# Optimization experiments

Hardware: AMD Instinct MI355X
Metric: run time of the kernel (lower is better)

## Reference

```python
import jax, jax.numpy as jnp
import numpy as np

D_MODEL = 1024
N_HEADS = 16
D_HEAD = D_MODEL // N_HEADS
B, T = 4, 2048


def setup_inputs() -> dict:
    key = jax.random.key(0)
    k1, k2, k3 = jax.random.split(key, 3)
    x = jax.random.normal(k1, (B, T, D_MODEL), dtype=jnp.float32)
    # match nn.Linear init scale roughly (uniform ~ 1/sqrt(fan_in)); scale normal for stability
    w_qkv = jax.random.normal(k2, (D_MODEL, 3 * D_MODEL), dtype=jnp.float32) / np.sqrt(D_MODEL)
    w_out = jax.random.normal(k3, (D_MODEL, D_MODEL), dtype=jnp.float32) / np.sqrt(D_MODEL)
    return {"x": x, "w_qkv": w_qkv, "w_out": w_out}


def reference(x, w_qkv, w_out):
    Bx, Tx, D = x.shape
    H, Dh = N_HEADS, D_HEAD
    qkv = x @ w_qkv                                  # [B,T,3D]
    qkv = qkv.reshape(Bx, Tx, 3, H, Dh)
    q, k, v = qkv[:, :, 0], qkv[:, :, 1], qkv[:, :, 2]  # [B,T,H,Dh]
    scores = jnp.einsum('bqhd,bkhd->bhqk', q, k) / np.sqrt(Dh).astype(np.float32)
    mask = jnp.triu(jnp.ones((Tx, Tx), dtype=bool), k=1)  # causal: mask future
    scores = jnp.where(mask, -jnp.inf, scores)
    attn = jax.nn.softmax(scores, axis=-1)
    out = jnp.einsum('bhqk,bkhd->bqhd', attn, v).reshape(Bx, Tx, D)
    return out @ w_out
```

## Files before the change

### kernel.cpp

```cpp
#include <hip/hip_runtime.h>
#include <math.h>

#define T_SEQ 2048
#define NB 4
#define NH 16
#define DH 64
#define DM 1024

typedef __attribute__((ext_vector_type(8))) __bf16 bf16x8;
typedef __attribute__((ext_vector_type(4))) float f32x4;

typedef const __attribute__((address_space(1))) void* gas_t;
typedef __attribute__((address_space(3))) void* las_t;

#if __has_builtin(__builtin_amdgcn_exp2f)
#define EXP2(x) __builtin_amdgcn_exp2f(x)
#else
#define EXP2(x) __expf((x) * 0.69314718056f)
#endif

#define SCHED0 __builtin_amdgcn_sched_barrier(0)
#define GLD(src, dst) __builtin_amdgcn_global_load_lds((gas_t)(src), (las_t)(dst), 16, 0, 0)
#define WAIT_VM(N) asm volatile("s_waitcnt vmcnt(" #N ")" ::: "memory")
#define WAIT_LGKM0 asm volatile("s_waitcnt lgkmcnt(0)" ::: "memory")
#define MEMFENCE   asm volatile("" ::: "memory")

__device__ inline bool detect_f32(const unsigned short* probe, int lane) {
    unsigned short u = probe[lane];
    int e = (u >> 7) & 0xFF;
    bool outlier = (e >= 140) || (e <= 90 && (u & 0x7fff) != 0);
    unsigned long long m = __ballot(outlier);
    return __popcll(m) >= 4;
}

__device__ inline bf16x8 load8_flex(const void* base, long elem, bool f32) {
    if (!f32) {
        return *(const bf16x8*)((const __bf16*)base + elem);
    } else {
        const float* f = (const float*)base + elem;
        float4 a = *(const float4*)f;
        float4 b = *(const float4*)(f + 4);
        bf16x8 r;
        r[0] = (__bf16)a.x; r[1] = (__bf16)a.y; r[2] = (__bf16)a.z; r[3] = (__bf16)a.w;
        r[4] = (__bf16)b.x; r[5] = (__bf16)b.y; r[6] = (__bf16)b.z; r[7] = (__bf16)b.w;
        return r;
    }
}

__global__ __launch_bounds__(256)
void cvt_x(const float* __restrict__ in, __bf16* __restrict__ out, long n8) {
    long i = (long)blockIdx.x * blockDim.x + threadIdx.x;
    if (i >= n8) return;
    const float* f = in + i * 8;
    float4 a = *(const float4*)f;
    float4 b = *(const float4*)(f + 4);
    bf16x8 r;
    r[0] = (__bf16)a.x; r[1] = (__bf16)a.y; r[2] = (__bf16)a.z; r[3] = (__bf16)a.w;
    r[4] = (__bf16)b.x; r[5] = (__bf16)b.y; r[6] = (__bf16)b.z; r[7] = (__bf16)b.w;
    *(bf16x8*)(out + i * 8) = r;
}

__global__ __launch_bounds__(256)
void tpose_cvt(const float* __restrict__ in, __bf16* __restrict__ out, int R, int C) {
    __shared__ __bf16 tile[32][33];
    const int bx = blockIdx.x * 32;
    const int by = blockIdx.y * 32;
    const int tx = threadIdx.x & 31;
    const int ty = threadIdx.x >> 5;
#pragma unroll
    for (int it = 0; it < 4; ++it) {
        int r = ty + it * 8;
        tile[r][tx] = (__bf16)in[(long)(by + r) * C + bx + tx];
    }
    __syncthreads();
#pragma unroll
    for (int it = 0; it < 4; ++it) {
        int r = ty + it * 8;
        out[(long)(bx + r) * R + by + tx] = tile[tx][r];
    }
}

__global__ __launch_bounds__(512, 2)
void gemm_8p(const __bf16* __restrict__ A, long lda,
             const __bf16* __restrict__ Bt, long ldb,
             void* __restrict__ C, long ldc, int c_f32, int K) {
    constexpr int AUNIT = 128 * 32;
    constexpr int BUNIT = 256 * 32;
    constexpr int UNIT  = AUNIT + BUNIT;
    __shared__ __align__(16) __bf16 lds[4 * UNIT];

    const int tid  = threadIdx.x;
    const int lane = tid & 63;
    const int wave = tid >> 6;
    const int l15  = lane & 15;
    const int quad = lane >> 4;

    const int wg   = blockIdx.x;
    const int xcd  = wg & 7;
    const int idx  = wg >> 3;
    const int bm   = (xcd * 8 + (idx & 7)) * 128;
    const int bn   = (idx >> 3) * 256;

    const int wm = (wave & 1) * 64;
    const int wn = (wave >> 1) * 64;

    f32x4 zero = {0.f, 0.f, 0.f, 0.f};
    f32x4 acc[4][4];
#pragma unroll
    for (int i = 0; i < 4; ++i)
#pragma unroll
        for (int j = 0; j < 4; ++j) acc[i][j] = zero;

    const int srow  = lane >> 2;
    const int swcol = ((lane & 3) ^ ((lane >> 3) & 3)) * 8;
    const __bf16* aS = A  + (long)(bm + wave * 16 + srow) * lda + swcol;
    const __bf16* bS = Bt + (long)(bn + wave * 32 + srow) * ldb + swcol;

    const int rsel = ((l15 >> 1) & 3);
    const int rcol = ((quad ^ rsel) * 8);

    const int NHALF = K >> 5;

#pragma unroll
    for (int u = 0; u < 3; ++u) {
        __bf16* wU = lds + u * UNIT;
        const long kc = (long)u * 32;
        GLD(aS + kc,            wU + wave * 512);
        GLD(bS + kc,            wU + AUNIT + (wave * 2 + 0) * 512);
        GLD(bS + 16 * ldb + kc, wU + AUNIT + (wave * 2 + 1) * 512);
    }
    SCHED0;
    WAIT_VM(6);
    SCHED0;
    __builtin_amdgcn_s_barrier();
    SCHED0;

    for (int h = 0; h < NHALF; ++h) {
        const __bf16* uA = lds + (h & 3) * UNIT;
        const __bf16* uB = uA + AUNIT;
        __bf16* wU = lds + ((h + 3) & 3) * UNIT;

        bf16x8 af[4], bf[4];
#pragma unroll
        for (int i = 0; i < 4; ++i)
            af[i] = *(const bf16x8*)(uA + (wm + i * 16 + l15) * 32 + rcol);
#pragma unroll
        for (int j = 0; j < 4; ++j)
            bf[j] = *(const bf16x8*)(uB + (wn + j * 16 + l15) * 32 + rcol);

        if (h + 3 < NHALF) {
            const long kc = (long)(h + 3) * 32;
            GLD(aS + kc,            wU + wave * 512);
            GLD(bS + kc,            wU + AUNIT + (wave * 2 + 0) * 512);
            GLD(bS + 16 * ldb + kc, wU + AUNIT + (wave * 2 + 1) * 512);
        }
        SCHED0;
        WAIT_LGKM0;
        SCHED0;
        __builtin_amdgcn_s_setprio(1);
#pragma unroll
        for (int i = 0; i < 4; ++i)
#pragma unroll
            for (int j = 0; j < 4; ++j)
                acc[i][j] = __builtin_amdgcn_mfma_f32_16x16x32_bf16(af[i], bf[j], acc[i][j], 0, 0, 0);
        __builtin_amdgcn_s_setprio(0);
        SCHED0;
        if (h < NHALF - 3)       WAIT_VM(6);
        else if (h == NHALF - 3) WAIT_VM(3);
        else                     WAIT_VM(0);
        SCHED0;
        MEMFENCE;
        __builtin_amdgcn_s_barrier();
        SCHED0;
    }

#pragma unroll
    for (int i = 0; i < 4; ++i)
#pragma unroll
        for (int j = 0; j < 4; ++j)
#pragma unroll
            for (int r = 0; r < 4; ++r) {
                int row = bm + wm + i * 16 + quad * 4 + r;
                int col = bn + wn + j * 16 + l15;
                if (c_f32)
                    ((float*)C)[(long)row * ldc + col] = acc[i][j][r];
                else
                    ((__bf16*)C)[(long)row * ldc + col] = (__bf16)acc[i][j][r];
            }
}

__global__ __launch_bounds__(256)
void gemm_bn(const void* __restrict__ A, long lda, long a0, int a_flex,
             const void* __restrict__ B, long ldb, int b_flex,
             void* __restrict__ C, long ldc, int c_flex, int K,
             const unsigned short* __restrict__ probe) {
    __shared__ __align__(16) __bf16 sA[128 * 32];
    __shared__ __align__(16) __bf16 sB[128 * 32];
    const int tid  = threadIdx.x;
    const int lane = tid & 63;
    const int wave = tid >> 6;
    const int l15  = lane & 15;
    const int quad = lane >> 4;
    const int bm = blockIdx.y * 128;
    const int bn = blockIdx.x * 128;
    const int wm = (wave & 1) * 64;
    const int wn = (wave >> 1) * 64;

    const bool is_f32 = detect_f32(probe, lane);
    const bool a_f32 = a_flex && is_f32;
    const bool b_f32 = b_flex && is_f32;
    const bool c_f32 = c_flex && is_f32;

    f32x4 zero = {0.f, 0.f, 0.f, 0.f};
    f32x4 acc[4][4];
#pragma unroll
    for (int i = 0; i < 4; ++i)
#pragma unroll
        for (int j = 0; j < 4; ++j) acc[i][j] = zero;

    const int srow = tid >> 2;
    const int scol = (tid & 3) * 8;

    for (int k0 = 0; k0 < K; k0 += 32) {
        __syncthreads();
        *(bf16x8*)(sA + tid * 8) =
            load8_flex(A, a0 + (long)(bm + srow) * lda + k0 + scol, a_f32);
        *(bf16x8*)(sA + 2048 + tid * 8) =
            load8_flex(A, a0 + (long)(bm + 64 + srow) * lda + k0 + scol, a_f32);
#pragma unroll
        for (int it = 0; it < 2; ++it) {
            int idx = tid + it * 256;
            int kk  = idx & 31;
            int n8  = (idx >> 5) * 8;
            bf16x8 bv = load8_flex(B, (long)(k0 + kk) * ldb + bn + n8, b_f32);
#pragma unroll
            for (int jj = 0; jj < 8; ++jj) sB[(n8 + jj) * 32 + kk] = bv[jj];
        }
        __syncthreads();

        bf16x8 af[4], bfm[4];
#pragma unroll
        for (int i = 0; i < 4; ++i)
            af[i] = *(const bf16x8*)(sA + (wm + i * 16 + l15) * 32 + quad * 8);
#pragma unroll
        for (int j = 0; j < 4; ++j)
            bfm[j] = *(const bf16x8*)(sB + (wn + j * 16 + l15) * 32 + quad * 8);
#pragma unroll
        for (int i = 0; i < 4; ++i)
#pragma unroll
            for (int j = 0; j < 4; ++j)
                acc[i][j] = __builtin_amdgcn_mfma_f32_16x16x32_bf16(af[i], bfm[j], acc[i][j], 0, 0, 0);
    }

#pragma unroll
    for (int i = 0; i < 4; ++i)
#pragma unroll
        for (int j = 0; j < 4; ++j)
#pragma unroll
            for (int r = 0; r < 4; ++r) {
                int row = bm + wm + i * 16 + quad * 4 + r;
                int col = bn + wn + j * 16 + l15;
                if (c_f32)
                    ((float*)C)[(long)row * ldc + col] = acc[i][j][r];
                else
                    ((__bf16*)C)[(long)row * ldc + col] = (__bf16)acc[i][j][r];
            }
}

__global__ __launch_bounds__(512, 4)
void attn_k(__bf16* __restrict__ qkvp, int bhbits) {
    const int bid  = blockIdx.x;
    const int p    = bid >> bhbits;
    const int bh   = bid & ((1 << bhbits) - 1);
    const int h    = bh & 15;
    const int b    = bh >> 4;
    const int tid  = threadIdx.x;
    const int lane = tid & 63;
    const int wave = tid >> 6;
    const int l15  = lane & 15;
    const int quad = lane >> 4;

    __shared__ __align__(16) __bf16 sK[64 * 72];
    __shared__ __align__(16) __bf16 sVT[64 * 64];
    __shared__ __align__(16) __bf16 sP[8][16 * 64];

    const long rs = 3 * DM;
    __bf16* base = qkvp + (long)b * T_SEQ * rs + h * DH;

    const int sr  = tid >> 3;
    const int sm  = tid & 7;
    const int sc8 = sm * 8;
    const int rot = 8 * ((5 * sm) & 7);
    const int vcol = (sr + rot) & 63;

    bf16x8 vone;
#pragma unroll
    for (int jj = 0; jj < 8; ++jj) vone[jj] = (__bf16)1.0f;

    f32x4 zero = {0.f, 0.f, 0.f, 0.f};

#pragma unroll 1
    for (int half = 0; half < 2; ++half) {
        const int qt  = half ? (15 - p) : p;
        const int q0  = qt * 128;
        const int wq0 = q0 + wave * 16;
        const int nk  = (q0 + 128) >> 6;

        const float qscale = 0.125f * 1.44269504089f;
        bf16x8 qa[2];
#pragma unroll
        for (int kk = 0; kk < 2; ++kk) {
            bf16x8 v = *(const bf16x8*)(base + (long)(wq0 + l15) * rs + kk * 32 + quad * 8);
#pragma unroll
            for (int jj = 0; jj < 8; ++jj) v[jj] = (__bf16)((float)v[jj] * qscale);
            qa[kk] = v;
        }

        f32x4 o[4], o4;
        o4 = zero;
#pragma unroll
        for (int j = 0; j < 4; ++j) o[j] = zero;

        bf16x8 kreg, vreg;
        {
            const __bf16* rp = base + (long)sr * rs;
            kreg = *(const bf16x8*)(rp + DM + sc8);
            vreg = *(const bf16x8*)(rp + 2 * DM + sc8);
        }

        for (int t = 0; t < nk; ++t) {
            const int k0 = t * 64;
            __syncthreads();
            *(bf16x8*)(sK + sr * 72 + sc8) = kreg;
#pragma unroll
            for (int jj = 0; jj < 8; ++jj)
                sVT[(sc8 + jj) * 64 + vcol] = vreg[jj];
            __syncthreads();

            if (t + 1 < nk) {
                const __bf16* rp = base + (long)(k0 + 64 + sr) * rs;
                kreg = *(const bf16x8*)(rp + DM + sc8);
                vreg = *(const bf16x8*)(rp + 2 * DM + sc8);
            }

            const bool active = (k0 <= wq0 + 15);
            if (active) {
                f32x4 s[4];
#pragma unroll
                for (int j = 0; j < 4; ++j) s[j] = zero;
#pragma unroll
                for (int kk = 0; kk < 2; ++kk) {
                    bf16x8 kb[4];
#pragma unroll
                    for (int j = 0; j < 4; ++j)
                        kb[j] = *(const bf16x8*)(sK + (j * 16 + l15) * 72 + kk * 32 + quad * 8);
#pragma unroll
                    for (int j = 0; j < 4; ++j)
                        s[j] = __builtin_amdgcn_mfma_f32_16x16x32_bf16(qa[kk], kb[j], s[j], 0, 0, 0);
                }

                const bool needmask = (k0 + 63 > wq0);
#pragma unroll
                for (int r = 0; r < 4; ++r) {
                    const int qg = wq0 + quad * 4 + r;
#pragma unroll
                    for (int j = 0; j < 4; ++j) {
                        const int kg = k0 + j * 16 + l15;
                        float pv = EXP2(fminf(s[j][r], 86.f));
                        if (needmask) pv = (kg > qg) ? 0.f : pv;
                        sP[wave][(quad * 4 + r) * 64 +
                                 ((j * 16 + l15 + 16 * quad) & 63)] = (__bf16)pv;
                    }
                }
            }

            SCHED0;
            WAIT_LGKM0;
            SCHED0;

            if (active) {
#pragma unroll
                for (int kk = 0; kk < 2; ++kk) {
                    bf16x8 pa, vb[4];
                    pa = *(const bf16x8*)(
                        &sP[wave][l15 * 64 +
                                  ((kk * 32 + quad * 8 + 16 * (l15 >> 2)) & 63)]);
#pragma unroll
                    for (int j = 0; j < 4; ++j) {
                        const int g = (2 * j + (l15 >> 3)) & 7;
                        vb[j] = *(const bf16x8*)(
                            sVT + (j * 16 + l15) * 64 +
                            ((kk * 32 + quad * 8 + 8 * ((5 * g) & 7)) & 63));
                    }
#pragma unroll
                    for (int j = 0; j < 4; ++j)
                        o[j] = __builtin_amdgcn_mfma_f32_16x16x32_bf16(pa, vb[j], o[j], 0, 0, 0);
                    o4 = __builtin_amdgcn_mfma_f32_16x16x32_bf16(pa, vone, o4, 0, 0, 0);
                }
            }
        }

#pragma unroll
        for (int r = 0; r < 4; ++r) {
            const int qg  = wq0 + quad * 4 + r;
            const float inv = 1.f / o4[r];
#pragma unroll
            for (int j = 0; j < 4; ++j)
                base[(long)qg * rs + j * 16 + l15] = (__bf16)(o[j][r] * inv);
        }
    }
}

__global__ __launch_bounds__(256)
void fallback_k(float* __restrict__ out, long n, float wsmb) {
    long i = (long)blockIdx.x * blockDim.x + threadIdx.x;
    for (; i < n; i += (long)gridDim.x * blockDim.x) out[i] = 0.f;
    if (blockIdx.x == 0 && threadIdx.x == 0) out[0] = wsmb;
}

extern "C" void kernel_launch(void* const* d_in, const int* in_sizes, int n_in,
                              void* d_out, int out_size, void* d_ws, size_t ws_size,
                              hipStream_t stream) {
    const void* x     = d_in[0];
    const void* w_qkv = d_in[1];
    const void* w_out = d_in[2];
    const unsigned short* probe = (const unsigned short*)d_in[0];

    __bf16* qkv = (__bf16*)d_ws;
    __bf16* xb  = qkv + (size_t)8192 * 3072;
    __bf16* wtq = xb  + (size_t)8192 * 1024;
    __bf16* wto = wtq + (size_t)3072 * 1024;

    const size_t NEED_T1   = (size_t)72 * 1024 * 1024;
    const size_t NEED_FULL = (size_t)8192 * 3072 * 2;
    const size_t NEED_B    = (size_t)2048 * 3072 * 2;

    if (ws_size >= NEED_T1) {
        cvt_x<<<dim3(4096), 256, 0, stream>>>((const float*)x, xb, (long)8192 * 1024 / 8);
        tpose_cvt<<<dim3(96, 32), 256, 0, stream>>>((const float*)w_qkv, wtq, 1024, 3072);
        tpose_cvt<<<dim3(32, 32), 256, 0, stream>>>((const float*)w_out, wto, 1024, 1024);
        gemm_8p<<<dim3(768), 512, 0, stream>>>(xb, 1024, wtq, 1024, qkv, 3072, 0, 1024);
        attn_k<<<dim3(8 * 64), 512, 0, stream>>>(qkv, 6);
        gemm_8p<<<dim3(256), 512, 0, stream>>>(qkv, 3072, wto, 1024, d_out, 1024, 1, 1024);
    } else if (ws_size >= NEED_FULL) {
        gemm_bn<<<dim3(24, 64), 256, 0, stream>>>(
            x, 1024, 0, 1, w_qkv, 3072, 1, qkv, 3072, 0, 1024, probe);
        attn_k<<<dim3(8 * 64), 512, 0, stream>>>(qkv, 6);
        gemm_bn<<<dim3(8, 64), 256, 0, stream>>>(
            qkv, 3072, 0, 0, w_out, 1024, 1, d_out, 1024, 1, 1024, probe);
    } else if (ws_size >= NEED_B) {
        for (int b = 0; b < NB; ++b) {
            long xoff = (long)b * T_SEQ * DM;
            gemm_bn<<<dim3(24, 16), 256, 0, stream>>>(
                x, 1024, xoff, 1, w_qkv, 3072, 1, qkv, 3072, 0, 1024, probe);
            attn_k<<<dim3(8 * 16), 512, 0, stream>>>(qkv, 4);
            gemm_bn<<<dim3(8, 16), 256, 0, stream>>>(
                qkv, 3072, 0, 0, w_out, 1024, 1,
                (void*)((char*)d_out + (size_t)b * T_SEQ * DM * 4),
                1024, 1, 1024, probe);
        }
    } else {
        fallback_k<<<dim3(512), 256, 0, stream>>>(
            (float*)d_out, (long)8192 * 1024, (float)(ws_size >> 20));
    }
}
```

Before: 259.7 us.

## Switch GEMM to 128x128 tiles with 4 waves and triple-buffered LDS

Replaces the 512-thread 128x256 GEMM tile with a 256-thread 128x128 tile. The LDS ring drops from four stages to three, prefetching two K-steps ahead, and the grid sizes for both projections double. The goal is smaller per-block LDS and more resident blocks per CU (launch bounds 3), improving occupancy and tail balance. The cost is less operand reuse per loaded byte and a shallower prefetch depth.

Result: no change. 256.5 us (-1.2%).

```diff
diff --git a/kernel.cpp b/kernel.cpp
--- a/kernel.cpp
+++ b/kernel.cpp
@@ -80,14 +80,13 @@
     }
 }
 
-__global__ __launch_bounds__(512, 2)
-void gemm_8p(const __bf16* __restrict__ A, long lda,
+__global__ __launch_bounds__(256, 3)
+void gemm_p3(const __bf16* __restrict__ A, long lda,
              const __bf16* __restrict__ Bt, long ldb,
              void* __restrict__ C, long ldc, int c_f32, int K) {
     constexpr int AUNIT = 128 * 32;
-    constexpr int BUNIT = 256 * 32;
-    constexpr int UNIT  = AUNIT + BUNIT;
-    __shared__ __align__(16) __bf16 lds[4 * UNIT];
+    constexpr int UNIT  = 2 * AUNIT;
+    __shared__ __align__(16) __bf16 lds[3 * UNIT];
 
     const int tid  = threadIdx.x;
     const int lane = tid & 63;
@@ -99,7 +98,7 @@
     const int xcd  = wg & 7;
     const int idx  = wg >> 3;
     const int bm   = (xcd * 8 + (idx & 7)) * 128;
-    const int bn   = (idx >> 3) * 256;
+    const int bn   = (idx >> 3) * 128;
 
     const int wm = (wave & 1) * 64;
     const int wn = (wave >> 1) * 64;
@@ -113,32 +112,33 @@
 
     const int srow  = lane >> 2;
     const int swcol = ((lane & 3) ^ ((lane >> 3) & 3)) * 8;
-    const __bf16* aS = A  + (long)(bm + wave * 16 + srow) * lda + swcol;
+    const __bf16* aS = A  + (long)(bm + wave * 32 + srow) * lda + swcol;
     const __bf16* bS = Bt + (long)(bn + wave * 32 + srow) * ldb + swcol;
 
-    const int rsel = ((l15 >> 1) & 3);
-    const int rcol = ((quad ^ rsel) * 8);
+    const int rcol = (quad ^ ((l15 >> 1) & 3)) * 8;
 
     const int NHALF = K >> 5;
 
 #pragma unroll
-    for (int u = 0; u < 3; ++u) {
+    for (int u = 0; u < 2; ++u) {
         __bf16* wU = lds + u * UNIT;
         const long kc = (long)u * 32;
-        GLD(aS + kc,            wU + wave * 512);
-        GLD(bS + kc,            wU + AUNIT + (wave * 2 + 0) * 512);
-        GLD(bS + 16 * ldb + kc, wU + AUNIT + (wave * 2 + 1) * 512);
+        GLD(aS + kc,            wU + wave * 1024);
+        GLD(aS + 16 * lda + kc, wU + wave * 1024 + 512);
+        GLD(bS + kc,            wU + AUNIT + wave * 1024);
+        GLD(bS + 16 * ldb + kc, wU + AUNIT + wave * 1024 + 512);
     }
     SCHED0;
-    WAIT_VM(6);
+    WAIT_VM(4);
     SCHED0;
     __builtin_amdgcn_s_barrier();
     SCHED0;
 
+    int cu = 0;
+    int su = 2;
     for (int h = 0; h < NHALF; ++h) {
-        const __bf16* uA = lds + (h & 3) * UNIT;
+        const __bf16* uA = lds + cu * UNIT;
         const __bf16* uB = uA + AUNIT;
-        __bf16* wU = lds + ((h + 3) & 3) * UNIT;
 
         bf16x8 af[4], bf[4];
 #pragma unroll
@@ -148,11 +148,13 @@
         for (int j = 0; j < 4; ++j)
             bf[j] = *(const bf16x8*)(uB + (wn + j * 16 + l15) * 32 + rcol);
 
-        if (h + 3 < NHALF) {
-            const long kc = (long)(h + 3) * 32;
-            GLD(aS + kc,            wU + wave * 512);
-            GLD(bS + kc,            wU + AUNIT + (wave * 2 + 0) * 512);
-            GLD(bS + 16 * ldb + kc, wU + AUNIT + (wave * 2 + 1) * 512);
+        if (h + 2 < NHALF) {
+            __bf16* wU = lds + su * UNIT;
+            const long kc = (long)(h + 2) * 32;
+            GLD(aS + kc,            wU + wave * 1024);
+            GLD(aS + 16 * lda + kc, wU + wave * 1024 + 512);
+            GLD(bS + kc,            wU + AUNIT + wave * 1024);
+            GLD(bS + 16 * ldb + kc, wU + AUNIT + wave * 1024 + 512);
         }
         SCHED0;
         WAIT_LGKM0;
@@ -165,13 +167,15 @@
                 acc[i][j] = __builtin_amdgcn_mfma_f32_16x16x32_bf16(af[i], bf[j], acc[i][j], 0, 0, 0);
         __builtin_amdgcn_s_setprio(0);
         SCHED0;
-        if (h < NHALF - 3)       WAIT_VM(6);
-        else if (h == NHALF - 3) WAIT_VM(3);
-        else                     WAIT_VM(0);
+        if (h < NHALF - 2) WAIT_VM(4);
+        else               WAIT_VM(0);
         SCHED0;
         MEMFENCE;
         __builtin_amdgcn_s_barrier();
         SCHED0;
+
+        cu = (cu == 2) ? 0 : cu + 1;
+        su = (su == 2) ? 0 : su + 1;
     }
 
 #pragma unroll
@@ -439,9 +443,9 @@
         cvt_x<<<dim3(4096), 256, 0, stream>>>((const float*)x, xb, (long)8192 * 1024 / 8);
         tpose_cvt<<<dim3(96, 32), 256, 0, stream>>>((const float*)w_qkv, wtq, 1024, 3072);
         tpose_cvt<<<dim3(32, 32), 256, 0, stream>>>((const float*)w_out, wto, 1024, 1024);
-        gemm_8p<<<dim3(768), 512, 0, stream>>>(xb, 1024, wtq, 1024, qkv, 3072, 0, 1024);
+        gemm_p3<<<dim3(1536), 256, 0, stream>>>(xb, 1024, wtq, 1024, qkv, 3072, 0, 1024);
         attn_k<<<dim3(8 * 64), 512, 0, stream>>>(qkv, 6);
-        gemm_8p<<<dim3(256), 512, 0, stream>>>(qkv, 3072, wto, 1024, d_out, 1024, 1, 1024);
+        gemm_p3<<<dim3(512), 256, 0, stream>>>(qkv, 3072, wto, 1024, d_out, 1024, 1, 1024);
     } else if (ws_size >= NEED_FULL) {
         gemm_bn<<<dim3(24, 64), 256, 0, stream>>>(
             x, 1024, 0, 1, w_qkv, 3072, 1, qkv, 3072, 0, 1024, probe);
```
